# Kernel optimization log

Hardware: AMD Instinct MI355X
Metric: run time of the kernel (lower is better)

## Reference

```python
import jax, jax.numpy as jnp
import numpy as np
import math

STATE_DIM = 256
R_MIN, R_MAX = 0.4, 0.9
PHASE_MAX = 2.0 * math.pi
BATCH, SEQ = 8, 4096


def setup_inputs() -> dict:
    key = jax.random.key(0)
    k_x, k_u1, k_u2, k_br, k_bi, k_cr, k_ci = jax.random.split(key, 7)
    D = STATE_DIM
    x = jax.random.normal(k_x, (BATCH, SEQ, D), dtype=jnp.float32)
    # parameter init mirroring the torch module
    u1 = jax.random.uniform(k_u1, (D,), dtype=jnp.float32)
    nu_log = jnp.log(-0.5 * jnp.log(u1 * (R_MAX + R_MIN) * (R_MAX - R_MIN) + R_MIN ** 2))
    u2 = jax.random.uniform(k_u2, (D,), dtype=jnp.float32)
    theta_log = jnp.log(PHASE_MAX * u2)
    lam_mod = jnp.exp(-jnp.exp(nu_log))
    gamma_log = jnp.log(jnp.sqrt(1.0 - jnp.square(lam_mod)))
    s_b = 1.0 / math.sqrt(2 * D)
    s_c = 1.0 / math.sqrt(D)
    B_re = jax.random.normal(k_br, (D, D), dtype=jnp.float32) * s_b
    B_im = jax.random.normal(k_bi, (D, D), dtype=jnp.float32) * s_b
    C_re = jax.random.normal(k_cr, (D, D), dtype=jnp.float32) * s_c
    C_im = jax.random.normal(k_ci, (D, D), dtype=jnp.float32) * s_c
    return {"x": x, "nu_log": nu_log, "theta_log": theta_log, "gamma_log": gamma_log,
            "B_re": B_re, "B_im": B_im, "C_re": C_re, "C_im": C_im}


def _binop(e_i, e_j):
    # diagonal linear recurrence composition: (a, b) -> h_t = a*h_{t-1} + b
    a_i, b_i = e_i
    a_j, b_j = e_j
    return a_j * a_i, a_j * b_i + b_j


def reference(x, nu_log, theta_log, gamma_log, B_re, B_im, C_re, C_im):
    L_mod = jnp.exp(-jnp.exp(nu_log))                       # [D]
    theta = jnp.exp(theta_log)
    L_diag = (L_mod * jnp.cos(theta) + 1j * L_mod * jnp.sin(theta)).astype(jnp.complex64)
    B = (B_re + 1j * B_im).astype(jnpp.complex64) if False else (B_re + 1j * B_im).astype(jnp.complex64)
    C = (C_re + 1j * C_im).astype(jnp.complex64)
    B_norm = B * jnp.exp(gamma_log)[:, None]                # [D, D] complex
    # input projection: [B, T, D] @ B_norm.T -> complex [B, T, D]
    B_elems = x.astype(jnp.complex64) @ B_norm.T
    L_elems = jnp.broadcast_to(L_diag, B_elems.shape)       # [B, T, D]
    # parallel associative scan over time axis
    _, inner_states = jax.lax.associative_scan(_binop, (L_elems, B_elems), axis=1)
    return (inner_states @ C.T).real                        # [B, T, D] float32
```

## Files before the change

### kernel.cpp

```cpp
#include <hip/hip_runtime.h>
#include <math.h>

#define D 256
#define NBATCH 8
#define T 4096
#define M (NBATCH * T)
#define LC 64
#define NC (T / LC)

typedef __attribute__((ext_vector_type(8))) short bf16x8;
typedef __attribute__((ext_vector_type(4))) float f32x4;

__device__ __forceinline__ unsigned short f2bf(float f) {
    unsigned int u = __float_as_uint(f);
    u += 0x7fff + ((u >> 16) & 1);
    return (unsigned short)(u >> 16);
}
__device__ __forceinline__ float bf2f(unsigned short s) {
    return __uint_as_float(((unsigned int)s) << 16);
}

__device__ __forceinline__ void gl_lds16(const unsigned short* g, unsigned short* l) {
    __builtin_amdgcn_global_load_lds(
        (const __attribute__((address_space(1))) unsigned int*)g,
        (__attribute__((address_space(3))) unsigned int*)l, 16, 0, 0);
}

__global__ void prep_params(const float* __restrict__ nu_log,
                            const float* __restrict__ theta_log,
                            float* __restrict__ Lr, float* __restrict__ Li) {
    int d = threadIdx.x;
    float lmod = expf(-expf(nu_log[d]));
    float th = expf(theta_log[d]);
    Lr[d] = lmod * cosf(th);
    Li[d] = lmod * sinf(th);
}

__global__ __launch_bounds__(256) void prep_w(const float* __restrict__ Bre,
                                              const float* __restrict__ Bim,
                                              const float* __restrict__ gamma_log,
                                              const float* __restrict__ Cre,
                                              const float* __restrict__ Cim,
                                              unsigned short* __restrict__ W2,
                                              unsigned short* __restrict__ W3) {
    int n = blockIdx.x, k = threadIdx.x;
    if (n < 512) {
        int r = n & 255;
        float g = expf(gamma_log[r]);
        const float* src = (n < 256) ? Bre : Bim;
        W2[(size_t)n * 256 + k] = f2bf(src[(size_t)r * 256 + k] * g);
    } else {
        int r = n - 512;
        W3[(size_t)r * 512 + k]       = f2bf(Cre[(size_t)r * 256 + k]);
        W3[(size_t)r * 512 + 256 + k] = f2bf(-Cim[(size_t)r * 256 + k]);
    }
}

__global__ __launch_bounds__(256) void proj_gemm(const float* __restrict__ x,
                                                 const unsigned short* __restrict__ W,
                                                 unsigned short* __restrict__ oU,
                                                 unsigned short* __restrict__ oV) {
    __shared__ __align__(16) unsigned short As[128 * 32];
    __shared__ __align__(16) unsigned short Bs[128 * 32];
    const int tid  = threadIdx.x;
    const int lane = tid & 63;
    const int wid  = tid >> 6;
    const int m0 = blockIdx.x * 128;
    const int n0 = blockIdx.y * 128;
    const int wr = wid >> 1, wc = wid & 1;

    f32x4 acc[4][4];
#pragma unroll
    for (int i = 0; i < 4; ++i)
#pragma unroll
        for (int j = 0; j < 4; ++j) acc[i][j] = (f32x4){0.f, 0.f, 0.f, 0.f};

    const int aq = tid & 7, arow = tid >> 3;
    const float* gx = x + (size_t)(m0 + arow) * 256 + aq * 4;
    unsigned short* lA = As + arow * 32 + aq * 4;
    const int sr = lane >> 2, sc = (lane & 3) * 8;
    const unsigned short* gW0 = W + (size_t)(n0 + wid * 32 + sr) * 256 + sc;
    const unsigned short* gW1 = gW0 + (size_t)16 * 256;
    unsigned short* lB0 = Bs + wid * 1024;
    unsigned short* lB1 = lB0 + 512;

    const int ar = lane & 15;
    const int ak = (lane >> 4) * 8;

    for (int k0 = 0; k0 < 256; k0 += 32) {
        gl_lds16(gW0 + k0, lB0);
        gl_lds16(gW1 + k0, lB1);
#pragma unroll
        for (int i = 0; i < 4; ++i) {
            float4 v = *(const float4*)(gx + (size_t)(32 * i) * 256 + k0);
            union { ushort4 s; unsigned long long u; } o;
            o.s.x = f2bf(v.x); o.s.y = f2bf(v.y); o.s.z = f2bf(v.z); o.s.w = f2bf(v.w);
            *(unsigned long long*)(lA + (size_t)i * 32 * 32) = o.u;
        }
        __syncthreads();
        bf16x8 a[4], b[4];
#pragma unroll
        for (int mi = 0; mi < 4; ++mi)
            a[mi] = *(const bf16x8*)(As + (wr * 64 + mi * 16 + ar) * 32 + ak);
#pragma unroll
        for (int ni = 0; ni < 4; ++ni)
            b[ni] = *(const bf16x8*)(Bs + (wc * 64 + ni * 16 + ar) * 32 + ak);
#pragma unroll
        for (int mi = 0; mi < 4; ++mi)
#pragma unroll
            for (int ni = 0; ni < 4; ++ni)
                acc[mi][ni] = __builtin_amdgcn_mfma_f32_16x16x32_bf16(a[mi], b[ni], acc[mi][ni], 0, 0, 0);
        __syncthreads();
    }

    const int crow = (lane >> 4) * 4;
    const int ccol = lane & 15;
    unsigned short* base = (n0 < 256) ? oU : oV;
    const int nb = (n0 < 256) ? n0 : (n0 - 256);
#pragma unroll
    for (int mi = 0; mi < 4; ++mi)
#pragma unroll
        for (int ni = 0; ni < 4; ++ni) {
            const int r = m0 + wr * 64 + mi * 16 + crow;
            const int c = nb + wc * 64 + ni * 16 + ccol;
#pragma unroll
            for (int j = 0; j < 4; ++j)
                base[(size_t)(r + j) * 256 + c] = f2bf(acc[mi][ni][j]);
        }
}

__global__ __launch_bounds__(256) void out_gemm(const unsigned short* __restrict__ A,
                                                const unsigned short* __restrict__ W,
                                                float* __restrict__ oF) {
    __shared__ __align__(16) unsigned short As[128 * 32];
    __shared__ __align__(16) unsigned short Bs[128 * 32];
    const int tid  = threadIdx.x;
    const int lane = tid & 63;
    const int wid  = tid >> 6;
    const int m0 = blockIdx.x * 128;
    const int n0 = blockIdx.y * 128;
    const int wr = wid >> 1, wc = wid & 1;

    f32x4 acc[4][4];
#pragma unroll
    for (int i = 0; i < 4; ++i)
#pragma unroll
        for (int j = 0; j < 4; ++j) acc[i][j] = (f32x4){0.f, 0.f, 0.f, 0.f};

    const int sr = lane >> 2;
    const int sc = (lane & 3) * 8;
    const unsigned short* gA0 = A + (size_t)(m0 + wid * 32 + sr) * 512 + sc;
    const unsigned short* gA1 = gA0 + (size_t)16 * 512;
    const unsigned short* gW0 = W + (size_t)(n0 + wid * 32 + sr) * 512 + sc;
    const unsigned short* gW1 = gW0 + (size_t)16 * 512;
    unsigned short* lA0 = As + wid * 1024;
    unsigned short* lA1 = lA0 + 512;
    unsigned short* lB0 = Bs + wid * 1024;
    unsigned short* lB1 = lB0 + 512;

    const int ar = lane & 15;
    const int ak = (lane >> 4) * 8;

    for (int k0 = 0; k0 < 512; k0 += 32) {
        gl_lds16(gA0 + k0, lA0);
        gl_lds16(gA1 + k0, lA1);
        gl_lds16(gW0 + k0, lB0);
        gl_lds16(gW1 + k0, lB1);
        __syncthreads();
        bf16x8 a[4], b[4];
#pragma unroll
        for (int mi = 0; mi < 4; ++mi)
            a[mi] = *(const bf16x8*)(As + (wr * 64 + mi * 16 + ar) * 32 + ak);
#pragma unroll
        for (int ni = 0; ni < 4; ++ni)
            b[ni] = *(const bf16x8*)(Bs + (wc * 64 + ni * 16 + ar) * 32 + ak);
#pragma unroll
        for (int mi = 0; mi < 4; ++mi)
#pragma unroll
            for (int ni = 0; ni < 4; ++ni)
                acc[mi][ni] = __builtin_amdgcn_mfma_f32_16x16x32_bf16(a[mi], b[ni], acc[mi][ni], 0, 0, 0);
        __syncthreads();
    }

    const int crow = (lane >> 4) * 4;
    const int ccol = lane & 15;
#pragma unroll
    for (int mi = 0; mi < 4; ++mi)
#pragma unroll
        for (int ni = 0; ni < 4; ++ni) {
            const int r = m0 + wr * 64 + mi * 16 + crow;
            const int c = n0 + wc * 64 + ni * 16 + ccol;
#pragma unroll
            for (int j = 0; j < 4; ++j)
                oF[(size_t)(r + j) * 256 + c] = acc[mi][ni][j];
        }
}

__global__ __launch_bounds__(256) void scan_ends(const unsigned short* __restrict__ Ub,
                                                 const unsigned short* __restrict__ Vb,
                                                 const float* __restrict__ Lr,
                                                 const float* __restrict__ Li,
                                                 float* __restrict__ cre, float* __restrict__ cim) {
    int d = threadIdx.x;
    int bc = blockIdx.x;
    float lr = Lr[d], li = Li[d];
    float hr = 0.f, hi = 0.f;
    size_t base = (size_t)bc * LC * 256 + d;
    for (int t = 0; t < LC; t++) {
        float u = bf2f(Ub[base + (size_t)t * 256]);
        float v = bf2f(Vb[base + (size_t)t * 256]);
        float nr = fmaf(lr, hr, fmaf(-li, hi, u));
        float ni = fmaf(lr, hi, fmaf(li, hr, v));
        hr = nr; hi = ni;
    }
    cre[(size_t)bc * 256 + d] = hr;
    cim[(size_t)bc * 256 + d] = hi;
}

__global__ __launch_bounds__(256) void scan_carry(float* __restrict__ cre, float* __restrict__ cim,
                                                  const float* __restrict__ Lr,
                                                  const float* __restrict__ Li) {
    int d = threadIdx.x;
    int b = blockIdx.x;
    float lr = Lr[d], li = Li[d];
    float ar = 1.f, ai = 0.f;
    for (int i = 0; i < LC; i++) {
        float nr = ar * lr - ai * li;
        float ni = ar * li + ai * lr;
        ar = nr; ai = ni;
    }
    float hr = 0.f, hi = 0.f;
    for (int c = 0; c < NC; c++) {
        size_t idx = ((size_t)b * NC + c) * 256 + d;
        float xr = cre[idx], xi = cim[idx];
        cre[idx] = hr;
        cim[idx] = hi;
        float nr = fmaf(ar, hr, fmaf(-ai, hi, xr));
        float ni = fmaf(ar, hi, fmaf(ai, hr, xi));
        hr = nr; hi = ni;
    }
}

__global__ __launch_bounds__(256) void scan_apply(const unsigned short* __restrict__ Ub,
                                                  const unsigned short* __restrict__ Vb,
                                                  const float* __restrict__ Lr,
                                                  const float* __restrict__ Li,
                                                  const float* __restrict__ cre,
                                                  const float* __restrict__ cim,
                                                  unsigned short* __restrict__ H) {
    int d = threadIdx.x;
    int bc = blockIdx.x;
    float lr = Lr[d], li = Li[d];
    float hr = cre[(size_t)bc * 256 + d];
    float hi = cim[(size_t)bc * 256 + d];
    size_t base  = (size_t)bc * LC * 256 + d;
    size_t hbase = (size_t)bc * LC * 512 + d;
    for (int t = 0; t < LC; t++) {
        float u = bf2f(Ub[base + (size_t)t * 256]);
        float v = bf2f(Vb[base + (size_t)t * 256]);
        float nr = fmaf(lr, hr, fmaf(-li, hi, u));
        float ni = fmaf(lr, hi, fmaf(li, hr, v));
        hr = nr; hi = ni;
        H[hbase + (size_t)t * 512]       = f2bf(hr);
        H[hbase + (size_t)t * 512 + 256] = f2bf(hi);
    }
}

extern "C" void kernel_launch(void* const* d_in, const int* in_sizes, int n_in,
                              void* d_out, int out_size, void* d_ws, size_t ws_size,
                              hipStream_t stream) {
    const float* x         = (const float*)d_in[0];
    const float* nu_log    = (const float*)d_in[1];
    const float* theta_log = (const float*)d_in[2];
    const float* gamma_log = (const float*)d_in[3];
    const float* B_re      = (const float*)d_in[4];
    const float* B_im      = (const float*)d_in[5];
    const float* C_re      = (const float*)d_in[6];
    const float* C_im      = (const float*)d_in[7];
    float* out = (float*)d_out;

    unsigned short* Ub = (unsigned short*)d_ws;
    unsigned short* Vb = Ub + (size_t)M * 256;
    unsigned short* H  = Vb + (size_t)M * 256;
    unsigned short* W2 = H + (size_t)M * 512;
    unsigned short* W3 = W2 + (size_t)512 * 256;
    float* cre = (float*)(W3 + (size_t)256 * 512);
    float* cim = cre + (size_t)NBATCH * NC * 256;
    float* Lr  = cim + (size_t)NBATCH * NC * 256;
    float* Li  = Lr + 256;

    prep_params<<<1, 256, 0, stream>>>(nu_log, theta_log, Lr, Li);
    prep_w<<<768, 256, 0, stream>>>(B_re, B_im, gamma_log, C_re, C_im, W2, W3);
    proj_gemm<<<dim3(M / 128, 4), 256, 0, stream>>>(x, W2, Ub, Vb);
    scan_ends<<<NBATCH * NC, 256, 0, stream>>>(Ub, Vb, Lr, Li, cre, cim);
    scan_carry<<<NBATCH, 256, 0, stream>>>(cre, cim, Lr, Li);
    scan_apply<<<NBATCH * NC, 256, 0, stream>>>(Ub, Vb, Lr, Li, cre, cim, H);
    out_gemm<<<dim3(M / 128, 2), 256, 0, stream>>>(H, W3, out);
}
```

Baseline: 79.24 us.

## Merge param prep kernels and fold chunk-carry scan into scan_apply

Merges prep_params into the weight-prep kernel as an extra block, and removes the serial scan_carry kernel. Each scan_apply block now recomputes its incoming carry by folding the chunk end-states of all earlier chunks in its batch. This removes two kernel launches and a latency-bound 8-block serial kernel. In exchange scan_apply does redundant O(NC) carry work per block, up to 63 extra global reads per thread.

```diff
diff --git a/kernel.cpp b/kernel.cpp
--- a/kernel.cpp
+++ b/kernel.cpp
@@ -26,33 +26,32 @@
         (__attribute__((address_space(3))) unsigned int*)l, 16, 0, 0);
 }
 
-__global__ void prep_params(const float* __restrict__ nu_log,
-                            const float* __restrict__ theta_log,
-                            float* __restrict__ Lr, float* __restrict__ Li) {
-    int d = threadIdx.x;
-    float lmod = expf(-expf(nu_log[d]));
-    float th = expf(theta_log[d]);
-    Lr[d] = lmod * cosf(th);
-    Li[d] = lmod * sinf(th);
-}
-
-__global__ __launch_bounds__(256) void prep_w(const float* __restrict__ Bre,
-                                              const float* __restrict__ Bim,
-                                              const float* __restrict__ gamma_log,
-                                              const float* __restrict__ Cre,
-                                              const float* __restrict__ Cim,
-                                              unsigned short* __restrict__ W2,
-                                              unsigned short* __restrict__ W3) {
+__global__ __launch_bounds__(256) void prep_all(const float* __restrict__ Bre,
+                                                const float* __restrict__ Bim,
+                                                const float* __restrict__ gamma_log,
+                                                const float* __restrict__ Cre,
+                                                const float* __restrict__ Cim,
+                                                const float* __restrict__ nu_log,
+                                                const float* __restrict__ theta_log,
+                                                unsigned short* __restrict__ W2,
+                                                unsigned short* __restrict__ W3,
+                                                float* __restrict__ Lr,
+                                                float* __restrict__ Li) {
     int n = blockIdx.x, k = threadIdx.x;
     if (n < 512) {
         int r = n & 255;
         float g = expf(gamma_log[r]);
         const float* src = (n < 256) ? Bre : Bim;
         W2[(size_t)n * 256 + k] = f2bf(src[(size_t)r * 256 + k] * g);
-    } else {
+    } else if (n < 768) {
         int r = n - 512;
         W3[(size_t)r * 512 + k]       = f2bf(Cre[(size_t)r * 256 + k]);
         W3[(size_t)r * 512 + 256 + k] = f2bf(-Cim[(size_t)r * 256 + k]);
+    } else {
+        float lmod = expf(-expf(nu_log[k]));
+        float th = expf(theta_log[k]);
+        Lr[k] = lmod * cosf(th);
+        Li[k] = lmod * sinf(th);
     }
 }
 
@@ -217,30 +216,6 @@
     cim[(size_t)bc * 256 + d] = hi;
 }
 
-__global__ __launch_bounds__(256) void scan_carry(float* __restrict__ cre, float* __restrict__ cim,
-                                                  const float* __restrict__ Lr,
-                                                  const float* __restrict__ Li) {
-    int d = threadIdx.x;
-    int b = blockIdx.x;
-    float lr = Lr[d], li = Li[d];
-    float ar = 1.f, ai = 0.f;
-    for (int i = 0; i < LC; i++) {
-        float nr = ar * lr - ai * li;
-        float ni = ar * li + ai * lr;
-        ar = nr; ai = ni;
-    }
-    float hr = 0.f, hi = 0.f;
-    for (int c = 0; c < NC; c++) {
-        size_t idx = ((size_t)b * NC + c) * 256 + d;
-        float xr = cre[idx], xi = cim[idx];
-        cre[idx] = hr;
-        cim[idx] = hi;
-        float nr = fmaf(ar, hr, fmaf(-ai, hi, xr));
-        float ni = fmaf(ar, hi, fmaf(ai, hr, xi));
-        hr = nr; hi = ni;
-    }
-}
-
 __global__ __launch_bounds__(256) void scan_apply(const unsigned short* __restrict__ Ub,
                                                   const unsigned short* __restrict__ Vb,
                                                   const float* __restrict__ Lr,
@@ -250,9 +225,23 @@
                                                   unsigned short* __restrict__ H) {
     int d = threadIdx.x;
     int bc = blockIdx.x;
+    int b = bc >> 6;
+    int c = bc & (NC - 1);
     float lr = Lr[d], li = Li[d];
-    float hr = cre[(size_t)bc * 256 + d];
-    float hi = cim[(size_t)bc * 256 + d];
+    float ar = 1.f, ai = 0.f;
+    for (int i = 0; i < LC; i++) {
+        float nr = ar * lr - ai * li;
+        float ni = ar * li + ai * lr;
+        ar = nr; ai = ni;
+    }
+    float hr = 0.f, hi = 0.f;
+    for (int cc = 0; cc < c; cc++) {
+        size_t idx = ((size_t)b * NC + cc) * 256 + d;
+        float er = cre[idx], ei = cim[idx];
+        float nr = fmaf(ar, hr, fmaf(-ai, hi, er));
+        float ni = fmaf(ar, hi, fmaf(ai, hr, ei));
+        hr = nr; hi = ni;
+    }
     size_t base  = (size_t)bc * LC * 256 + d;
     size_t hbase = (size_t)bc * LC * 512 + d;
     for (int t = 0; t < LC; t++) {
@@ -289,11 +278,10 @@
     float* Lr  = cim + (size_t)NBATCH * NC * 256;
     float* Li  = Lr + 256;
 
-    prep_params<<<1, 256, 0, stream>>>(nu_log, theta_log, Lr, Li);
-    prep_w<<<768, 256, 0, stream>>>(B_re, B_im, gamma_log, C_re, C_im, W2, W3);
+    prep_all<<<769, 256, 0, stream>>>(B_re, B_im, gamma_log, C_re, C_im,
+                                      nu_log, theta_log, W2, W3, Lr, Li);
     proj_gemm<<<dim3(M / 128, 4), 256, 0, stream>>>(x, W2, Ub, Vb);
     scan_ends<<<NBATCH * NC, 256, 0, stream>>>(Ub, Vb, Lr, Li, cre, cim);
-    scan_carry<<<NBATCH, 256, 0, stream>>>(cre, cim, Lr, Li);
     scan_apply<<<NBATCH * NC, 256, 0, stream>>>(Ub, Vb, Lr, Li, cre, cim, H);
     out_gemm<<<dim3(M / 128, 2), 256, 0, stream>>>(H, W3, out);
 }
```

New measurement: 84.91 us. +7.2%, slower.

## Pack U/V in 4-timestep groups, interleave H re/im, merge prep kernels

Applied to the files above, without the earlier changes.

The projection GEMM now writes U and V in a layout where each group of 4 consecutive timesteps for a channel is stored contiguously. The GEMM stores 8-byte vectors instead of scattered 2-byte writes, and the scan kernels load 4 timesteps per 8-byte read. The scan writes hidden states with real and imaginary parts interleaved as one 32-bit word, and the C weight matrix is interleaved to match. The two parameter-prep kernels are merged into one launch. This targets narrow strided memory accesses and one launch, at the cost of a coupled layout contract across the GEMMs and scans.

```diff
diff --git a/kernel.cpp b/kernel.cpp
--- a/kernel.cpp
+++ b/kernel.cpp
@@ -26,40 +26,39 @@
         (__attribute__((address_space(3))) unsigned int*)l, 16, 0, 0);
 }
 
-__global__ void prep_params(const float* __restrict__ nu_log,
-                            const float* __restrict__ theta_log,
-                            float* __restrict__ Lr, float* __restrict__ Li) {
-    int d = threadIdx.x;
-    float lmod = expf(-expf(nu_log[d]));
-    float th = expf(theta_log[d]);
-    Lr[d] = lmod * cosf(th);
-    Li[d] = lmod * sinf(th);
-}
-
-__global__ __launch_bounds__(256) void prep_w(const float* __restrict__ Bre,
-                                              const float* __restrict__ Bim,
-                                              const float* __restrict__ gamma_log,
-                                              const float* __restrict__ Cre,
-                                              const float* __restrict__ Cim,
-                                              unsigned short* __restrict__ W2,
-                                              unsigned short* __restrict__ W3) {
+__global__ __launch_bounds__(256) void prep_all(const float* __restrict__ Bre,
+                                                const float* __restrict__ Bim,
+                                                const float* __restrict__ gamma_log,
+                                                const float* __restrict__ Cre,
+                                                const float* __restrict__ Cim,
+                                                const float* __restrict__ nu_log,
+                                                const float* __restrict__ theta_log,
+                                                unsigned short* __restrict__ W2,
+                                                unsigned short* __restrict__ W3i,
+                                                float* __restrict__ Lr,
+                                                float* __restrict__ Li) {
     int n = blockIdx.x, k = threadIdx.x;
     if (n < 512) {
         int r = n & 255;
         float g = expf(gamma_log[r]);
         const float* src = (n < 256) ? Bre : Bim;
         W2[(size_t)n * 256 + k] = f2bf(src[(size_t)r * 256 + k] * g);
+    } else if (n < 768) {
+        int r = n - 512;
+        W3i[(size_t)r * 512 + 2 * k]     = f2bf(Cre[(size_t)r * 256 + k]);
+        W3i[(size_t)r * 512 + 2 * k + 1] = f2bf(-Cim[(size_t)r * 256 + k]);
     } else {
-        int r = n - 512;
-        W3[(size_t)r * 512 + k]       = f2bf(Cre[(size_t)r * 256 + k]);
-        W3[(size_t)r * 512 + 256 + k] = f2bf(-Cim[(size_t)r * 256 + k]);
+        float lmod = expf(-expf(nu_log[k]));
+        float th = expf(theta_log[k]);
+        Lr[k] = lmod * cosf(th);
+        Li[k] = lmod * sinf(th);
     }
 }
 
 __global__ __launch_bounds__(256) void proj_gemm(const float* __restrict__ x,
                                                  const unsigned short* __restrict__ W,
-                                                 unsigned short* __restrict__ oU,
-                                                 unsigned short* __restrict__ oV) {
+                                                 unsigned short* __restrict__ U4,
+                                                 unsigned short* __restrict__ V4) {
     __shared__ __align__(16) unsigned short As[128 * 32];
     __shared__ __align__(16) unsigned short Bs[128 * 32];
     const int tid  = threadIdx.x;
@@ -115,17 +114,18 @@
 
     const int crow = (lane >> 4) * 4;
     const int ccol = lane & 15;
-    unsigned short* base = (n0 < 256) ? oU : oV;
+    unsigned short* base = (n0 < 256) ? U4 : V4;
     const int nb = (n0 < 256) ? n0 : (n0 - 256);
 #pragma unroll
     for (int mi = 0; mi < 4; ++mi)
 #pragma unroll
         for (int ni = 0; ni < 4; ++ni) {
-            const int r = m0 + wr * 64 + mi * 16 + crow;
+            const int rg = (m0 + wr * 64 + mi * 16 + crow) >> 2;
             const int c = nb + wc * 64 + ni * 16 + ccol;
-#pragma unroll
-            for (int j = 0; j < 4; ++j)
-                base[(size_t)(r + j) * 256 + c] = f2bf(acc[mi][ni][j]);
+            uint2 o;
+            o.x = (unsigned int)f2bf(acc[mi][ni][0]) | ((unsigned int)f2bf(acc[mi][ni][1]) << 16);
+            o.y = (unsigned int)f2bf(acc[mi][ni][2]) | ((unsigned int)f2bf(acc[mi][ni][3]) << 16);
+            *(uint2*)(base + ((size_t)rg * 256 + c) * 4) = o;
         }
 }
 
@@ -196,8 +196,8 @@
         }
 }
 
-__global__ __launch_bounds__(256) void scan_ends(const unsigned short* __restrict__ Ub,
-                                                 const unsigned short* __restrict__ Vb,
+__global__ __launch_bounds__(256) void scan_ends(const unsigned short* __restrict__ U4,
+                                                 const unsigned short* __restrict__ V4,
                                                  const float* __restrict__ Lr,
                                                  const float* __restrict__ Li,
                                                  float* __restrict__ cre, float* __restrict__ cim) {
@@ -205,13 +205,19 @@
     int bc = blockIdx.x;
     float lr = Lr[d], li = Li[d];
     float hr = 0.f, hi = 0.f;
-    size_t base = (size_t)bc * LC * 256 + d;
-    for (int t = 0; t < LC; t++) {
-        float u = bf2f(Ub[base + (size_t)t * 256]);
-        float v = bf2f(Vb[base + (size_t)t * 256]);
-        float nr = fmaf(lr, hr, fmaf(-li, hi, u));
-        float ni = fmaf(lr, hi, fmaf(li, hr, v));
-        hr = nr; hi = ni;
+    for (int q = 0; q < 16; ++q) {
+        size_t eidx = ((size_t)(bc * 16 + q) * 256 + d) * 4;
+        uint2 uu = *(const uint2*)(U4 + eidx);
+        uint2 vv = *(const uint2*)(V4 + eidx);
+        unsigned int uw[2] = {uu.x, uu.y}, vw[2] = {vv.x, vv.y};
+#pragma unroll
+        for (int j = 0; j < 4; ++j) {
+            float u = bf2f((unsigned short)(uw[j >> 1] >> ((j & 1) * 16)));
+            float v = bf2f((unsigned short)(vw[j >> 1] >> ((j & 1) * 16)));
+            float nr = fmaf(lr, hr, fmaf(-li, hi, u));
+            float ni = fmaf(lr, hi, fmaf(li, hr, v));
+            hr = nr; hi = ni;
+        }
     }
     cre[(size_t)bc * 256 + d] = hr;
     cim[(size_t)bc * 256 + d] = hi;
@@ -241,28 +247,33 @@
     }
 }
 
-__global__ __launch_bounds__(256) void scan_apply(const unsigned short* __restrict__ Ub,
-                                                  const unsigned short* __restrict__ Vb,
+__global__ __launch_bounds__(256) void scan_apply(const unsigned short* __restrict__ U4,
+                                                  const unsigned short* __restrict__ V4,
                                                   const float* __restrict__ Lr,
                                                   const float* __restrict__ Li,
                                                   const float* __restrict__ cre,
                                                   const float* __restrict__ cim,
-                                                  unsigned short* __restrict__ H) {
+                                                  unsigned int* __restrict__ H32) {
     int d = threadIdx.x;
     int bc = blockIdx.x;
     float lr = Lr[d], li = Li[d];
     float hr = cre[(size_t)bc * 256 + d];
     float hi = cim[(size_t)bc * 256 + d];
-    size_t base  = (size_t)bc * LC * 256 + d;
-    size_t hbase = (size_t)bc * LC * 512 + d;
-    for (int t = 0; t < LC; t++) {
-        float u = bf2f(Ub[base + (size_t)t * 256]);
-        float v = bf2f(Vb[base + (size_t)t * 256]);
-        float nr = fmaf(lr, hr, fmaf(-li, hi, u));
-        float ni = fmaf(lr, hi, fmaf(li, hr, v));
-        hr = nr; hi = ni;
-        H[hbase + (size_t)t * 512]       = f2bf(hr);
-        H[hbase + (size_t)t * 512 + 256] = f2bf(hi);
+    for (int q = 0; q < 16; ++q) {
+        size_t eidx = ((size_t)(bc * 16 + q) * 256 + d) * 4;
+        uint2 uu = *(const uint2*)(U4 + eidx);
+        uint2 vv = *(const uint2*)(V4 + eidx);
+        unsigned int uw[2] = {uu.x, uu.y}, vw[2] = {vv.x, vv.y};
+#pragma unroll
+        for (int j = 0; j < 4; ++j) {
+            float u = bf2f((unsigned short)(uw[j >> 1] >> ((j & 1) * 16)));
+            float v = bf2f((unsigned short)(vw[j >> 1] >> ((j & 1) * 16)));
+            float nr = fmaf(lr, hr, fmaf(-li, hi, u));
+            float ni = fmaf(lr, hi, fmaf(li, hr, v));
+            hr = nr; hi = ni;
+            H32[(size_t)(bc * 64 + q * 4 + j) * 256 + d] =
+                (unsigned int)f2bf(hr) | ((unsigned int)f2bf(hi) << 16);
+        }
     }
 }
 
@@ -279,21 +290,22 @@
     const float* C_im      = (const float*)d_in[7];
     float* out = (float*)d_out;
 
-    unsigned short* Ub = (unsigned short*)d_ws;
-    unsigned short* Vb = Ub + (size_t)M * 256;
-    unsigned short* H  = Vb + (size_t)M * 256;
+    unsigned short* U4 = (unsigned short*)d_ws;
+    unsigned short* V4 = U4 + (size_t)M * 256;
+    unsigned short* H  = V4 + (size_t)M * 256;
     unsigned short* W2 = H + (size_t)M * 512;
-    unsigned short* W3 = W2 + (size_t)512 * 256;
-    float* cre = (float*)(W3 + (size_t)256 * 512);
+    unsigned short* W3i = W2 + (size_t)512 * 256;
+    float* cre = (float*)(W3i + (size_t)256 * 512);
     float* cim = cre + (size_t)NBATCH * NC * 256;
     float* Lr  = cim + (size_t)NBATCH * NC * 256;
     float* Li  = Lr + 256;
 
-    prep_params<<<1, 256, 0, stream>>>(nu_log, theta_log, Lr, Li);
-    prep_w<<<768, 256, 0, stream>>>(B_re, B_im, gamma_log, C_re, C_im, W2, W3);
-    proj_gemm<<<dim3(M / 128, 4), 256, 0, stream>>>(x, W2, Ub, Vb);
-    scan_ends<<<NBATCH * NC, 256, 0, stream>>>(Ub, Vb, Lr, Li, cre, cim);
+    prep_all<<<769, 256, 0, stream>>>(B_re, B_im, gamma_log, C_re, C_im,
+                                      nu_log, theta_log, W2, W3i, Lr, Li);
+    proj_gemm<<<dim3(M / 128, 4), 256, 0, stream>>>(x, W2, U4, V4);
+    scan_ends<<<NBATCH * NC, 256, 0, stream>>>(U4, V4, Lr, Li, cre, cim);
     scan_carry<<<NBATCH, 256, 0, stream>>>(cre, cim, Lr, Li);
-    scan_apply<<<NBATCH * NC, 256, 0, stream>>>(Ub, Vb, Lr, Li, cre, cim, H);
-    out_gemm<<<dim3(M / 128, 2), 256, 0, stream>>>(H, W3, out);
-}
+    scan_apply<<<NBATCH * NC, 256, 0, stream>>>(U4, V4, Lr, Li, cre, cim,
+                                                (unsigned int*)H);
+    out_gemm<<<dim3(M / 128, 2), 256, 0, stream>>>(H, W3i, out);
+}
```

After: 76.32 us. 1.04x faster.
